# Performance work log

Hardware: AMD Instinct MI355X
Metric: run time of the kernel (lower is better)

## Reference

```python
import jax, jax.numpy as jnp
import numpy as np

CONF_THRES = 0.5   # self.conf_thres
NMS_THRES = 0.5    # self.nms_thres
PRE_NMS = 2048     # candidates kept before pairwise IoU
MAX_DET = 300      # padded detections returned per image
MAX_WH = 4096.0    # class-offset trick so NMS is per-class
IMG_SIZE = 416.0   # self.img_size; boxes_scale (416,416)->(416,416) => scale 1


def xywh2xyxy(b):
    xy, wh = b[..., :2], b[..., 2:4]
    return jnp.concatenate([xy - wh * 0.5, xy + wh * 0.5], axis=-1)


def pairwise_iou(boxes):
    # boxes: [K,4] xyxy -> [K,K] IoU
    area = (boxes[:, 2] - boxes[:, 0]) * (boxes[:, 3] - boxes[:, 1])
    lt = jnp.maximum(boxes[:, None, :2], boxes[None, :, :2])
    rb = jnp.minimum(boxes[:, None, 2:], boxes[None, :, 2:])
    wh = jnp.clip(rb - lt, 0.0)
    inter = wh[..., 0] * wh[..., 1]
    return inter / (area[:, None] + area[None, :] - inter + 1e-16)


def nms_single(pred):
    # pred: [N,85] = xywh(4) + objectness(1) + class scores(80)
    boxes = xywh2xyxy(pred[:, :4])
    obj = pred[:, 4]
    cls_scores = pred[:, 5:] * obj[:, None]        # conf = obj * class prob
    conf = jnp.max(cls_scores, axis=-1)
    cls_id = jnp.argmax(cls_scores, axis=-1)
    valid = obj >= CONF_THRES                      # confidence threshold filter
    score = jnp.where(valid, conf, -1.0)

    order = jnp.argsort(-score)[:PRE_NMS]          # sort desc, keep top PRE_NMS
    boxes_s = boxes[order]
    score_s = score[order]
    cls_s = cls_id[order]
    valid_s = valid[order]

    # per-class NMS via coordinate offset by class id
    off = cls_s.astype(boxes_s.dtype) * MAX_WH
    iou = pairwise_iou(boxes_s + off[:, None])     # [PRE_NMS, PRE_NMS]

    def body(keep, i):
        suppressed = jnp.any(keep & (iou[:, i] > NMS_THRES))
        k = valid_s[i] & ~suppressed
        return keep.at[i].set(k), k

    keep, _ = jax.lax.scan(body, jnp.zeros(PRE_NMS, dtype=bool), jnp.arange(PRE_NMS))

    final_score = jnp.where(keep, score_s, -1.0)
    top = jnp.argsort(-final_score)[:MAX_DET]
    kb, ks, kc, km = boxes_s[top], score_s[top], cls_s[top], keep[top]

    scale = IMG_SIZE / 416.0                       # boxes_scale (identity here)
    det = jnp.concatenate(
        [kb * scale, ks[:, None], kc[:, None].astype(kb.dtype)], axis=-1)
    return jnp.where(km[:, None], det, 0.0)        # [MAX_DET, 6] padded


def setup_inputs() -> dict:
    key = jax.random.key(0)
    predictions = jax.random.uniform(key, (16, 10647, 85), dtype=jnp.float32)
    return {"predictions": predictions}


def reference(predictions):
    # detections per image: [x1,y1,x2,y2,score,class], zero-padded to MAX_DET
    return jax.vmap(nms_single)(predictions)  # [B, MAX_DET, 6]
```

## Files before the change

### kernel.cpp

```cpp
#include <hip/hip_runtime.h>
#include <hip/hip_bf16.h>
#include <stdint.h>

typedef unsigned long long u64;
typedef unsigned int u32;
typedef unsigned short u16;

#define NANCH 10647
#define NBATCH 16
#define NSORT 16384
#define NSEL 2048
#define NWORD 32
#define NCLS 80
#define CONF_T 0.5f
#define NMS_T 0.5f
#define MAXDET 300
#define MAXWH 4096.0f
#define CANDCAP 10688

__global__ __launch_bounds__(256) void k_prep(const float* __restrict__ pred,
                                              u64* __restrict__ keys,
                                              float4* __restrict__ boxes,
                                              int* __restrict__ cls,
                                              float* __restrict__ score,
                                              u32* __restrict__ ghist) {
    __shared__ float sm[128 * 85];
    __shared__ u32 ph[256];
    int b = blockIdx.y;
    int a0 = blockIdx.x * 128;
    int na = NANCH - a0; if (na > 128) na = 128;
    const float* src = pred + ((size_t)b * NANCH + a0) * 85;
    int tot = na * 85;
    ph[threadIdx.x] = 0;
    for (int i = threadIdx.x; i < tot; i += 256) sm[i] = src[i];
    __syncthreads();
    int t = threadIdx.x;
    u64 kk = 0;
    if (t < na) {
        const float* s = &sm[t * 85];
        float x = s[0], y = s[1], w = s[2], h = s[3], obj = s[4];
        float best = s[5] * obj; int arg = 0;
        #pragma unroll
        for (int c = 1; c < 80; ++c) {
            float v = s[5 + c] * obj;
            if (v > best) { best = v; arg = c; }
        }
        bool valid = obj >= CONF_T;
        float sc = valid ? best : -1.0f;
        int a = a0 + t;
        float4 bx;
        bx.x = x - w * 0.5f; bx.y = y - h * 0.5f;
        bx.z = x + w * 0.5f; bx.w = y + h * 0.5f;
        size_t o = (size_t)b * NANCH + a;
        boxes[o] = bx;
        cls[o] = arg;
        score[o] = sc;
        u32 u = __float_as_uint(sc);
        u32 v = (u & 0x80000000u) ? ~u : (u | 0x80000000u);
        u32 hi = ~v;
        kk = ((u64)hi << 32) | (u32)a;
        keys[(size_t)b * NSORT + a] = kk;
    }
    u32 bin = (t < na) ? (u32)(kk >> 56) : 0xFFFFFFFFu;
    int lane = t & 63;
    u64 rem = __ballot(t < na);
    while (rem) {
        int srcl = __ffsll((long long)rem) - 1;
        u32 lb = __shfl(bin, srcl);
        u64 same = __ballot(bin == lb) & rem;
        if (lane == srcl) atomicAdd(&ph[lb], (u32)__popcll(same));
        rem &= ~same;
    }
    __syncthreads();
    if (ph[threadIdx.x]) atomicAdd(&ghist[(size_t)b * 256 + threadIdx.x], ph[threadIdx.x]);
}

__global__ __launch_bounds__(1024) void k_sel(const u64* __restrict__ keys,
                                              const u32* __restrict__ ghist,
                                              const float4* __restrict__ boxes,
                                              const int* __restrict__ cls,
                                              const float* __restrict__ score,
                                              float4* __restrict__ sel_box,
                                              float4* __restrict__ sel_sbox,
                                              float* __restrict__ sel_area,
                                              float* __restrict__ sel_score,
                                              int* __restrict__ sel_cls) {
    __shared__ u64 sk[NSEL];
    __shared__ u64 cand[CANDCAP];
    __shared__ u32 hist[256];
    __shared__ u32 hsc[256];
    __shared__ u64 s_red[16];
    __shared__ u32 s_D0, s_D, s_rank, s_cnt, s_cand;

    int b = blockIdx.x;
    int tid = threadIdx.x;
    int lane = tid & 63;
    u64 below = (1ULL << lane) - 1ULL;
    const u64* KB = keys + (size_t)b * NSORT;

    if (tid == 0) { s_cnt = 0; s_cand = 0; }
    for (int i = tid; i < NSEL; i += 1024) sk[i] = ~0ULL;
    if (tid < 256) hist[tid] = ghist[(size_t)b * 256 + tid];
    __syncthreads();
    if (tid < 64) {
        u32 h0 = hist[tid*4], h1 = hist[tid*4+1], h2 = hist[tid*4+2], h3 = hist[tid*4+3];
        u32 loc = h0 + h1 + h2 + h3;
        u32 p = loc;
        #pragma unroll
        for (int o = 1; o < 64; o <<= 1) { u32 t2 = __shfl_up(p, o); if (lane >= o) p += t2; }
        u32 base = p - loc;
        hsc[tid*4]   = base + h0;
        hsc[tid*4+1] = base + h0 + h1;
        hsc[tid*4+2] = base + h0 + h1 + h2;
        hsc[tid*4+3] = base + h0 + h1 + h2 + h3;
    }
    __syncthreads();
    if (tid < 256) {
        u32 inc = hsc[tid], cb = inc - hist[tid];
        if (cb < NSEL && NSEL <= inc) { s_D0 = tid; s_rank = NSEL - cb; }
    }
    __syncthreads();
    u32 D0 = s_D0;

    for (int it = 0; it < 11; ++it) {
        int i = tid + it * 1024;
        bool inb = i < NANCH;
        u64 kk = inb ? KB[i] : 0ULL;
        u32 top = (u32)(kk >> 56);
        bool is_s = inb && (top < D0);
        bool is_c = inb && (top == D0);
        u64 bs = __ballot(is_s), bc = __ballot(is_c);
        u32 base_s = 0, base_c = 0;
        if (lane == 0) {
            if (bs) base_s = atomicAdd(&s_cnt, (u32)__popcll(bs));
            if (bc) base_c = atomicAdd(&s_cand, (u32)__popcll(bc));
        }
        base_s = __shfl(base_s, 0); base_c = __shfl(base_c, 0);
        if (is_s) sk[base_s + __popcll(bs & below)] = kk;
        if (is_c) cand[base_c + __popcll(bc & below)] = kk;
    }
    __syncthreads();

    const int shifts2[5] = {48, 40, 32, 8, 0};
    for (int rr = 0; ; ++rr) {
        u32 cn = s_cand, r = s_rank;
        if (r == cn || rr == 5) {
            for (u32 i0 = 0; i0 < cn; i0 += 1024) {
                u32 i = i0 + tid;
                bool take = i < cn;
                u64 kk = take ? cand[i] : 0ULL;
                u64 bt = __ballot(take);
                u32 base = 0;
                if (lane == 0 && bt) base = atomicAdd(&s_cnt, (u32)__popcll(bt));
                base = __shfl(base, 0);
                if (take) sk[base + __popcll(bt & below)] = kk;
            }
            break;
        }
        if (r == 1) {
            u64 best = ~0ULL;
            for (u32 i = tid; i < cn; i += 1024) { u64 kk = cand[i]; if (kk < best) best = kk; }
            #pragma unroll
            for (int o = 32; o > 0; o >>= 1) {
                u64 other = __shfl_down(best, o);
                if (other < best) best = other;
            }
            if (lane == 0) s_red[tid >> 6] = best;
            __syncthreads();
            if (tid == 0) {
                u64 m = s_red[0];
                for (int w2 = 1; w2 < 16; ++w2) if (s_red[w2] < m) m = s_red[w2];
                sk[atomicAdd(&s_cnt, 1u)] = m;
            }
            break;
        }
        int shift = shifts2[rr];
        if (tid < 256) hist[tid] = 0;
        __syncthreads();
        for (u32 i = tid; i < cn; i += 1024)
            atomicAdd(&hist[(u32)(cand[i] >> shift) & 0xFFu], 1u);
        __syncthreads();
        if (tid < 64) {
            u32 h0 = hist[tid*4], h1 = hist[tid*4+1], h2 = hist[tid*4+2], h3 = hist[tid*4+3];
            u32 loc = h0 + h1 + h2 + h3;
            u32 p = loc;
            #pragma unroll
            for (int o = 1; o < 64; o <<= 1) { u32 t2 = __shfl_up(p, o); if (lane >= o) p += t2; }
            u32 base = p - loc;
            hsc[tid*4]   = base + h0;
            hsc[tid*4+1] = base + h0 + h1;
            hsc[tid*4+2] = base + h0 + h1 + h2;
            hsc[tid*4+3] = base + h0 + h1 + h2 + h3;
        }
        __syncthreads();
        if (tid < 256) {
            u32 inc = hsc[tid], cb = inc - hist[tid];
            if (cb < r && r <= inc) { s_D = tid; s_rank = r - cb; }
        }
        __syncthreads();
        u32 D = s_D;
        u64 mk[11], mc[11]; int nk = 0, nc = 0;
        for (u32 i = tid; i < cn; i += 1024) {
            u64 kk = cand[i];
            u32 dg = (u32)(kk >> shift) & 0xFFu;
            if (dg < D) mk[nk++] = kk;
            else if (dg == D) mc[nc++] = kk;
        }
        __syncthreads();
        if (tid == 0) s_cand = 0;
        __syncthreads();
        if (nk) { u32 p = atomicAdd(&s_cnt, (u32)nk); for (int j = 0; j < nk; ++j) sk[p + j] = mk[j]; }
        if (nc) { u32 p = atomicAdd(&s_cand, (u32)nc); for (int j = 0; j < nc; ++j) cand[p + j] = mc[j]; }
        __syncthreads();
    }
    __syncthreads();

    for (int k = 2; k <= NSEL; k <<= 1) {
        for (int j = k >> 1; j > 0; j >>= 1) {
            int n = tid;
            int i = ((n & ~(j - 1)) << 1) | (n & (j - 1));
            int l = i | j;
            u64 a = sk[i], c = sk[l];
            bool up = ((i & k) == 0);
            if ((a > c) == up) { sk[i] = c; sk[l] = a; }
            __syncthreads();
        }
    }

    for (int r2 = tid; r2 < NSEL; r2 += 1024) {
        u64 key = sk[r2];
        int a = (int)(key & 0xFFFFFFFFu);
        if ((unsigned)a >= NANCH) a = 0;
        size_t src = (size_t)b * NANCH + a;
        float4 bx = boxes[src];
        int c = cls[src];
        float sc = score[src];
        float off = (float)c * MAXWH;
        float4 sb;
        sb.x = bx.x + off; sb.y = bx.y + off;
        sb.z = bx.z + off; sb.w = bx.w + off;
        float area = (sb.z - sb.x) * (sb.w - sb.y);
        size_t o = (size_t)b * NSEL + r2;
        sel_box[o] = bx; sel_sbox[o] = sb; sel_area[o] = area;
        sel_score[o] = sc; sel_cls[o] = c;
    }
}

__global__ __launch_bounds__(1024) void k_cnms(const float4* __restrict__ sel_sbox,
                                               const float* __restrict__ sel_area,
                                               const int* __restrict__ sel_cls,
                                               const float* __restrict__ sel_score,
                                               u64* __restrict__ gkeep) {
    __shared__ u16 wmem[16][NSEL];
    __shared__ u64 wkeep[16][NWORD];

    int b = blockIdx.y;
    int cg = blockIdx.x;
    int lane = threadIdx.x & 63, wv = threadIdx.x >> 6;
    int c = cg * 16 + wv;
    size_t bb = (size_t)b * NSEL;
    const int* CL = sel_cls + bb;
    const float* SC = sel_score + bb;
    u64 below = (1ULL << lane) - 1ULL;

    int n = 0;
    for (int ch = 0; ch < NWORD; ++ch) {
        int i = ch * 64 + lane;
        bool pred = (CL[i] == c) && (SC[i] >= 0.0f);
        u64 bal = __ballot(pred);
        if (pred) wmem[wv][n + __popcll(bal & below)] = (u16)i;
        n += __popcll(bal);
    }

    for (int c0 = 0; c0 < n; c0 += 64) {
        int chunkn = n - c0; if (chunkn > 64) chunkn = 64;
        bool mv = lane < chunkn;
        int q = mv ? (int)wmem[wv][c0 + lane] : 0;
        float4 bq = sel_sbox[bb + q];
        float aq = sel_area[bb + q];

        bool hit = false;
        for (int j = 0; j < c0; ++j) {
            if (!((wkeep[wv][j >> 6] >> (j & 63)) & 1ULL)) continue;
            int p = (int)wmem[wv][j];
            float4 bp = sel_sbox[bb + p];
            float ap = sel_area[bb + p];
            float ltx = fmaxf(bp.x, bq.x), lty = fmaxf(bp.y, bq.y);
            float rbx = fminf(bp.z, bq.z), rby = fminf(bp.w, bq.w);
            float ww = fmaxf(rbx - ltx, 0.0f), hh = fmaxf(rby - lty, 0.0f);
            float inter = ww * hh;
            hit = hit || (mv && (inter / (ap + aq - inter + 1e-16f) > NMS_T));
        }
        u64 avail = __ballot(mv && !hit);

        u64 Rt = 0;
        for (int t = 0; t < chunkn; ++t) {
            int p = (int)wmem[wv][c0 + t];
            float4 bp = sel_sbox[bb + p];
            float ap = sel_area[bb + p];
            float ltx = fmaxf(bp.x, bq.x), lty = fmaxf(bp.y, bq.y);
            float rbx = fminf(bp.z, bq.z), rby = fminf(bp.w, bq.w);
            float ww = fmaxf(rbx - ltx, 0.0f), hh = fmaxf(rby - lty, 0.0f);
            float inter = ww * hh;
            u64 row = __ballot(mv && (inter / (ap + aq - inter + 1e-16f) > NMS_T));
            if (lane == t) Rt = row;
        }

        u64 U = avail, kept = 0;
        while (U) {
            bool inU = ((U >> lane) & 1ULL) != 0ULL;
            u64 newk = __ballot(inU && ((Rt & U & below) == 0ULL));
            u64 killed = __ballot((Rt & newk) != 0ULL);
            kept |= newk;
            U &= ~(newk | killed);
        }
        if (lane == 0) wkeep[wv][c0 >> 6] = kept;
        if ((kept >> lane) & 1ULL)
            atomicOr(&gkeep[(size_t)b * NWORD + (q >> 6)], 1ULL << (q & 63));
    }
}

__global__ __launch_bounds__(64) void k_out(const u64* __restrict__ gkeep,
                                            const float4* __restrict__ sel_box,
                                            const float* __restrict__ sel_score,
                                            const int* __restrict__ sel_cls,
                                            float* __restrict__ out) {
    int b = blockIdx.x;
    int lane = threadIdx.x;
    const float* SC = sel_score + (size_t)b * NSEL;
    u64 kreg = (lane < NWORD) ? gkeep[(size_t)b * NWORD + lane] : 0ULL;

    int cnt = (lane < NWORD) ? __popcll(kreg) : 0;
    int pre = cnt;
    #pragma unroll
    for (int dd = 1; dd < 64; dd <<= 1) {
        int o = __shfl_up(pre, dd);
        if (lane >= dd) pre += o;
    }
    int total = __shfl(pre, 63);
    int base = pre - cnt;
    float* OUT = out + (size_t)b * MAXDET * 6;
    if (lane < NWORD) {
        u64 m = kreg;
        int rr = 0;
        while (m) {
            int t = __ffsll((long long)m) - 1;
            m &= m - 1;
            int slot = base + rr; ++rr;
            if (slot < MAXDET) {
                int i = lane * 64 + t;
                size_t src = (size_t)b * NSEL + i;
                float4 bx = sel_box[src];
                float sc = SC[i];
                int c = sel_cls[src];
                float* o6 = OUT + slot * 6;
                o6[0] = bx.x; o6[1] = bx.y; o6[2] = bx.z; o6[3] = bx.w;
                o6[4] = sc; o6[5] = (float)c;
            }
        }
    }
    int start = total > MAXDET ? MAXDET : total;
    for (int s = start + lane; s < MAXDET; s += 64) {
        float* o6 = OUT + s * 6;
        o6[0] = 0.0f; o6[1] = 0.0f; o6[2] = 0.0f;
        o6[3] = 0.0f; o6[4] = 0.0f; o6[5] = 0.0f;
    }
}

extern "C" void kernel_launch(void* const* d_in, const int* in_sizes, int n_in,
                              void* d_out, int out_size, void* d_ws, size_t ws_size,
                              hipStream_t stream) {
    const float* pred = (const float*)d_in[0];
    float* out = (float*)d_out;

    char* ws = (char*)d_ws;
    size_t off = 0;
    auto alloc = [&](size_t bytes) -> void* {
        void* p = ws + off;
        off += (bytes + 255) & ~(size_t)255;
        return p;
    };

    u64*    keys      = (u64*)   alloc((size_t)NBATCH * NSORT * 8);
    float4* boxes     = (float4*)alloc((size_t)NBATCH * NANCH * 16);
    int*    cls       = (int*)   alloc((size_t)NBATCH * NANCH * 4);
    float*  score     = (float*) alloc((size_t)NBATCH * NANCH * 4);
    float4* sel_box   = (float4*)alloc((size_t)NBATCH * NSEL * 16);
    float4* sel_sbox  = (float4*)alloc((size_t)NBATCH * NSEL * 16);
    float*  sel_area  = (float*) alloc((size_t)NBATCH * NSEL * 4);
    float*  sel_score = (float*) alloc((size_t)NBATCH * NSEL * 4);
    int*    sel_cls   = (int*)   alloc((size_t)NBATCH * NSEL * 4);
    u64*    gkeep     = (u64*)   alloc((size_t)NBATCH * NWORD * 8);
    u32*    ghist     = (u32*)   alloc((size_t)NBATCH * 256 * 4);

    hipMemsetAsync(gkeep, 0, (size_t)NBATCH * NWORD * 8 + (size_t)NBATCH * 256 * 4, stream);

    dim3 g1((NANCH + 127) / 128, NBATCH);
    k_prep<<<g1, 256, 0, stream>>>(pred, keys, boxes, cls, score, ghist);

    k_sel<<<NBATCH, 1024, 0, stream>>>(keys, ghist, boxes, cls, score,
                                       sel_box, sel_sbox, sel_area,
                                       sel_score, sel_cls);

    dim3 g3(5, NBATCH);
    k_cnms<<<g3, 1024, 0, stream>>>(sel_sbox, sel_area, sel_cls, sel_score, gkeep);

    k_out<<<NBATCH, 64, 0, stream>>>(gkeep, sel_box, sel_score, sel_cls, out);
}
```

Measured before the change: 109.0 us.

## Use register/shuffle bitonic stages in selection sort and replace memset with zero kernel

The bitonic sort of the 2048 selected keys now keeps two elements per lane in registers and does every stage with stride 64 or less through wavefront shuffles, with no shared-memory round trip or block barrier. Only the strides of 128 and above still go through shared memory with __syncthreads. The aim is to remove most of the 66 block-wide barriers and their LDS traffic. The hipMemsetAsync is also replaced by a small zeroing kernel to avoid memset launch overhead. The cost is more intricate direction logic, which risks ordering bugs.

```diff
diff --git a/kernel.cpp b/kernel.cpp
--- a/kernel.cpp
+++ b/kernel.cpp
@@ -17,6 +17,10 @@
 #define MAXDET 300
 #define MAXWH 4096.0f
 #define CANDCAP 10688
+
+__global__ __launch_bounds__(1024) void k_zero(u32* __restrict__ p, int nwords) {
+    for (int i = threadIdx.x; i < nwords; i += 1024) p[i] = 0;
+}
 
 __global__ __launch_bounds__(256) void k_prep(const float* __restrict__ pred,
                                               u64* __restrict__ keys,
@@ -215,14 +219,59 @@
     }
     __syncthreads();
 
-    for (int k = 2; k <= NSEL; k <<= 1) {
-        for (int j = k >> 1; j > 0; j >>= 1) {
-            int n = tid;
-            int i = ((n & ~(j - 1)) << 1) | (n & (j - 1));
-            int l = i | j;
-            u64 a = sk[i], c = sk[l];
-            bool up = ((i & k) == 0);
-            if ((a > c) == up) { sk[i] = c; sk[l] = a; }
+    {
+        int w = tid >> 6, l = lane;
+        int base = w * 128;
+        u64 a = sk[base + l], c = sk[base + 64 + l];
+        #pragma unroll
+        for (int k = 2; k <= 128; k <<= 1) {
+            for (int j = k >> 1; j > 0; j >>= 1) {
+                if (j == 64) {
+                    bool dir = (((base + l) & k) == 0);
+                    u64 lo = a < c ? a : c;
+                    u64 hi = a < c ? c : a;
+                    a = dir ? lo : hi;
+                    c = dir ? hi : lo;
+                } else {
+                    bool up_ = (l & j) != 0;
+                    bool dira = (((base + l) & k) == 0);
+                    bool dirc = (((base + 64 + l) & k) == 0);
+                    u64 pa = __shfl_xor(a, j);
+                    u64 pc = __shfl_xor(c, j);
+                    a = (up_ == dira) ? (a > pa ? a : pa) : (a < pa ? a : pa);
+                    c = (up_ == dirc) ? (c > pc ? c : pc) : (c < pc ? c : pc);
+                }
+            }
+        }
+        sk[base + l] = a; sk[base + 64 + l] = c;
+        __syncthreads();
+        for (int k = 256; k <= NSEL; k <<= 1) {
+            for (int j = k >> 1; j >= 128; j >>= 1) {
+                int n = tid;
+                int i = ((n & ~(j - 1)) << 1) | (n & (j - 1));
+                int l2 = i | j;
+                u64 x = sk[i], y = sk[l2];
+                bool up2 = ((i & k) == 0);
+                if ((x > y) == up2) { sk[i] = y; sk[l2] = x; }
+                __syncthreads();
+            }
+            a = sk[base + l]; c = sk[base + 64 + l];
+            bool dirk = ((base & k) == 0);
+            {
+                u64 lo = a < c ? a : c;
+                u64 hi = a < c ? c : a;
+                a = dirk ? lo : hi;
+                c = dirk ? hi : lo;
+            }
+            #pragma unroll
+            for (int j = 32; j > 0; j >>= 1) {
+                bool up_ = (l & j) != 0;
+                u64 pa = __shfl_xor(a, j);
+                u64 pc = __shfl_xor(c, j);
+                a = (up_ == dirk) ? (a > pa ? a : pa) : (a < pa ? a : pa);
+                c = (up_ == dirk) ? (c > pc ? c : pc) : (c < pc ? c : pc);
+            }
+            sk[base + l] = a; sk[base + 64 + l] = c;
             __syncthreads();
         }
     }
@@ -393,7 +442,8 @@
     u64*    gkeep     = (u64*)   alloc((size_t)NBATCH * NWORD * 8);
     u32*    ghist     = (u32*)   alloc((size_t)NBATCH * 256 * 4);
 
-    hipMemsetAsync(gkeep, 0, (size_t)NBATCH * NWORD * 8 + (size_t)NBATCH * 256 * 4, stream);
+    int zwords = (int)(((size_t)NBATCH * NWORD * 8 + (size_t)NBATCH * 256 * 4) / 4);
+    k_zero<<<1, 1024, 0, stream>>>((u32*)gkeep, zwords);
 
     dim3 g1((NANCH + 127) / 128, NBATCH);
     k_prep<<<g1, 256, 0, stream>>>(pred, keys, boxes, cls, score, ghist);
```

Result: no change. 109.4 us (+0.3%).
